# Kernel optimization log

Hardware: AMD Instinct MI355X
Metric: run time of the kernel (lower is better)

The kernel has to match this reference:

```python
import jax, jax.numpy as jnp
import numpy as np

N_QUBITS = 4
N_LAYERS = 2
BATCH = 524288


def _apply_1q(state, U, wire, batched):
    """Apply a 2x2 gate U on `wire`. state: [B,2,2,2,2]; U: [B,2,2] if batched else [2,2]."""
    ax = wire + 1
    s = jnp.moveaxis(state, ax, 1)
    if batched:
        s = jnp.einsum('bij,bj...->bi...', U, s)
    else:
        s = jnp.einsum('ij,bj...->bi...', U, s)
    return jnp.moveaxis(s, 1, ax)


def _apply_cnot(state, control, target):
    cax, tax = control + 1, target + 1
    s0 = jnp.take(state, 0, axis=cax)
    s1 = jnp.take(state, 1, axis=cax)
    t_ax = tax - 1 if tax > cax else tax  # target axis after removing control axis
    s1 = jnp.flip(s1, axis=t_ax)
    return jnp.stack([s0, s1], axis=cax)


def _circuit(x, weight):
    B = x.shape[0]
    # Angle encoding: RY(tanh(x_i) * pi) per wire (per-sample angles)
    theta = jnp.tanh(x) * jnp.pi  # [B, 4]
    state = jnp.zeros((B,) + (2,) * N_QUBITS, jnp.complex64)
    state = state.at[(slice(None),) + (0,) * N_QUBITS].set(1.0)
    for q in range(N_QUBITS):
        h = theta[:, q] * 0.5
        c, s = jnp.cos(h), jnp.sin(h)
        Ury = jnp.stack([jnp.stack([c, -s], -1), jnp.stack([s, c], -1)], -2).astype(jnp.complex64)  # [B,2,2]
        state = _apply_1q(state, Ury, q, batched=True)
    for layer in range(N_LAYERS):
        for q in range(N_QUBITS):
            hy = weight[layer, q, 0] * 0.5
            cy, sy = jnp.cos(hy), jnp.sin(hy)
            Uy = jnp.stack([jnp.stack([cy, -sy]), jnp.stack([sy, cy])]).astype(jnp.complex64)
            state = _apply_1q(state, Uy, q, batched=False)
            hz = weight[layer, q, 1] * 0.5
            ez = jnp.exp(-1j * hz.astype(jnp.complex64))
            z0 = jnp.zeros((), jnp.complex64)
            Uz = jnp.stack([jnp.stack([ez, z0]), jnp.stack([z0, jnp.conj(ez)])])
            state = _apply_1q(state, Uz, q, batched=False)
        for q in range(N_QUBITS):
            state = _apply_cnot(state, q, (q + 1) % N_QUBITS)
    # <Z_i> = P(bit_i = 0) - P(bit_i = 1)
    probs = jnp.abs(state) ** 2  # [B,2,2,2,2] float32
    outs = []
    for q in range(N_QUBITS):
        other_axes = tuple(a for a in range(1, N_QUBITS + 1) if a != q + 1)
        marg = probs.sum(other_axes)  # [B,2]
        outs.append(marg[:, 0] - marg[:, 1])
    return jnp.stack(outs, axis=-1).astype(jnp.float32)  # [B,4]


def setup_inputs() -> dict:
    key = jax.random.key(0)
    kx, kw = jax.random.split(key)
    x = jax.random.normal(kx, (BATCH, N_QUBITS), dtype=jnp.float32)
    weight = jax.random.normal(kw, (N_LAYERS, N_QUBITS, 2), dtype=jnp.float32) * 0.1
    return {"x": x, "weight": weight}


def reference(x, weight):
    return _circuit(x, weight)
```

## Files before the change

kernel.cpp:

```cpp
#include <hip/hip_runtime.h>
#include <math.h>


typedef _Float16 f16x4 __attribute__((ext_vector_type(4)));
typedef _Float16 f16x8 __attribute__((ext_vector_type(8)));
typedef float f32x4 __attribute__((ext_vector_type(4)));

static __device__ inline unsigned pk16(float a, float b) {
    unsigned short ua = __builtin_bit_cast(unsigned short, (_Float16)a);
    unsigned short ub = __builtin_bit_cast(unsigned short, (_Float16)b);
    return (unsigned)ua | ((unsigned)ub << 16);
}

__global__ __launch_bounds__(64) void build_U(
    const float* __restrict__ weight,
    uint2* __restrict__ UF)
{
    __shared__ float cw[16], sw[16];
    __shared__ float Ur[16][16], Ui[16][16];

    const int tid = threadIdx.x;
    if (tid < 16) {
        float h = 0.5f * weight[tid];
        __sincosf(h, &sw[tid], &cw[tid]);
    }
    __syncthreads();

    if (tid < 16) {
        const int col = tid;
        float re[16], im[16];
        #pragma unroll
        for (int i = 0; i < 16; ++i) { re[i] = 0.f; im[i] = 0.f; }
        re[col] = 1.f;

        #pragma unroll
        for (int layer = 0; layer < 2; ++layer) {
            #pragma unroll
            for (int q = 0; q < 4; ++q) {
                float cy = cw[layer*8 + q*2 + 0];
                float sy = sw[layer*8 + q*2 + 0];
                float cz = cw[layer*8 + q*2 + 1];
                float sz = sw[layer*8 + q*2 + 1];
                int st = 8 >> q;
                #pragma unroll
                for (int i = 0; i < 16; ++i) {
                    if (i & st) continue;
                    int j = i | st;
                    float r0 = re[i], r1 = re[j], i0 = im[i], i1 = im[j];
                    float nr0 = cy*r0 - sy*r1;
                    float nr1 = sy*r0 + cy*r1;
                    float ni0 = cy*i0 - sy*i1;
                    float ni1 = sy*i0 + cy*i1;
                    re[i] = nr0*cz + ni0*sz;
                    im[i] = ni0*cz - nr0*sz;
                    re[j] = nr1*cz - ni1*sz;
                    im[j] = ni1*cz + nr1*sz;
                }
            }
            #pragma unroll
            for (int q = 0; q < 4; ++q) {
                int cb = 8 >> q;
                int tb = 8 >> ((q + 1) & 3);
                #pragma unroll
                for (int i = 0; i < 16; ++i) {
                    if ((i & cb) && !(i & tb)) {
                        int j = i | tb;
                        float tr = re[i]; re[i] = re[j]; re[j] = tr;
                        float ti = im[i]; im[i] = im[j]; im[j] = ti;
                    }
                }
            }
        }
        #pragma unroll
        for (int i = 0; i < 16; ++i) { Ur[i][col] = re[i]; Ui[i][col] = im[i]; }
    }
    __syncthreads();

    {
        int m = tid & 15, k0 = (tid >> 4) << 2;
        UF[tid]      = uint2{pk16(Ur[m][k0], Ur[m][k0+1]),
                             pk16(Ur[m][k0+2], Ur[m][k0+3])};
        UF[64 + tid] = uint2{pk16(Ui[m][k0], Ui[m][k0+1]),
                             pk16(Ui[m][k0+2], Ui[m][k0+3])};
    }
}

__global__ __launch_bounds__(256) void qmain(
    const float* __restrict__ x,
    const uint2* __restrict__ UF,
    float* __restrict__ out,
    int B)
{
    __shared__ _Float16 S[256][16];

    const int tid  = threadIdx.x;
    const int lane = tid & 63;
    const int s0   = blockIdx.x * 256 + tid;

    float4 xv = (s0 < B) ? reinterpret_cast<const float4*>(x)[s0]
                         : float4{0.f, 0.f, 0.f, 0.f};

    uint2 ur2 = UF[lane];
    uint2 ui2 = UF[64 + lane];

    float c[4], s[4];
    {
        float xs[4] = {xv.x, xv.y, xv.z, xv.w};
        #pragma unroll
        for (int q = 0; q < 4; ++q) {
            float e = __expf(2.f * xs[q]);
            float uu = __builtin_amdgcn_rcpf(e + 1.f);
            float rr = 0.5f * uu;
            c[q] = __builtin_amdgcn_sinf(rr);
            s[q] = __builtin_amdgcn_cosf(rr);
        }
    }
    float a4[4] = {c[0]*c[1], c[0]*s[1], s[0]*c[1], s[0]*s[1]};
    float b4[4] = {c[2]*c[3], c[2]*s[3], s[2]*c[3], s[2]*s[3]};

    f16x8 lo, hi;
    #pragma unroll
    for (int i = 0; i < 8; ++i)  lo[i] = (_Float16)(a4[i >> 2] * b4[i & 3]);
    #pragma unroll
    for (int i = 8; i < 16; ++i) hi[i - 8] = (_Float16)(a4[i >> 2] * b4[i & 3]);
    *reinterpret_cast<f16x8*>(&S[tid][0]) = lo;
    *reinterpret_cast<f16x8*>(&S[tid][8]) = hi;
    __syncthreads();

    f16x4 afr = __builtin_bit_cast(f16x4, ur2);
    f16x4 afi = __builtin_bit_cast(f16x4, ui2);

    const int lg = lane >> 4;
    const int n  = lane & 15;
    const float sg1 = (lg & 1) ? -1.f : 1.f;
    const float sg0 = (lg & 2) ? -1.f : 1.f;
    const int wrow = tid & 192;
    const int wbase = blockIdx.x * 256 + wrow;

    #pragma unroll
    for (int g = 0; g < 4; ++g) {
        f16x4 bf = *reinterpret_cast<const f16x4*>(&S[wrow + g*16 + n][lg << 2]);

        f32x4 zero = {0.f, 0.f, 0.f, 0.f};
        f32x4 dre = __builtin_amdgcn_mfma_f32_16x16x16f16(afr, bf, zero, 0, 0, 0);
        f32x4 dim = __builtin_amdgcn_mfma_f32_16x16x16f16(afi, bf, zero, 0, 0, 0);

        float m0 = dre[0]*dre[0] + dim[0]*dim[0];
        float m1 = dre[1]*dre[1] + dim[1]*dim[1];
        float m2 = dre[2]*dre[2] + dim[2]*dim[2];
        float m3 = dre[3]*dre[3] + dim[3]*dim[3];

        float sum = (m0 + m1) + (m2 + m3);
        float z3 = (m0 - m1) + (m2 - m3);
        float z2 = (m0 + m1) - (m2 + m3);
        float z1 = sg1 * sum;
        float z0 = sg0 * sum;

        z0 += __shfl_xor(z0, 16); z0 += __shfl_xor(z0, 32);
        z1 += __shfl_xor(z1, 16); z1 += __shfl_xor(z1, 32);
        z2 += __shfl_xor(z2, 16); z2 += __shfl_xor(z2, 32);
        z3 += __shfl_xor(z3, 16); z3 += __shfl_xor(z3, 32);

        int samp = wbase + g*16 + n;
        if (lg == g && samp < B)
            reinterpret_cast<float4*>(out)[samp] = float4{z0, z1, z2, z3};
    }
}

extern "C" void kernel_launch(void* const* d_in, const int* in_sizes, int n_in,
                              void* d_out, int out_size, void* d_ws, size_t ws_size,
                              hipStream_t stream) {
    const float* x = (const float*)d_in[0];
    const float* w = (const float*)d_in[1];
    float* out = (float*)d_out;
    uint2* UF = (uint2*)d_ws;
    int B = in_sizes[0] / 4;

    build_U<<<1, 64, 0, stream>>>(w, UF);
    int grid = (B + 255) / 256;
    qmain<<<grid, 256, 0, stream>>>(x, UF, out, B);
}
```

Before: 68.71 us.

## Fuse unitary build into main kernel and reduce expectations with MFMA

Removes the separate single-block build_U launch, and has every block recompute the 16x16 circuit unitary in LDS from the weights, using 16 threads. The state layout in shared memory becomes column-major f16x4 slabs. The shuffle-based Z-expectation reduction is replaced by a third MFMA against a constant ±1 sign matrix, applied to f16 probabilities. This trades an extra kernel launch and a global round-trip for redundant per-block unitary computation on 16 serial threads, and adds f16 rounding of the probabilities.

```diff
diff --git a/kernel.cpp b/kernel.cpp
--- a/kernel.cpp
+++ b/kernel.cpp
@@ -3,28 +3,49 @@
 
 
 typedef _Float16 f16x4 __attribute__((ext_vector_type(4)));
-typedef _Float16 f16x8 __attribute__((ext_vector_type(8)));
 typedef float f32x4 __attribute__((ext_vector_type(4)));
 
-static __device__ inline unsigned pk16(float a, float b) {
-    unsigned short ua = __builtin_bit_cast(unsigned short, (_Float16)a);
-    unsigned short ub = __builtin_bit_cast(unsigned short, (_Float16)b);
-    return (unsigned)ua | ((unsigned)ub << 16);
-}
+__global__ __launch_bounds__(256, 8) void qfused(
+    const float* __restrict__ x,
+    const float* __restrict__ weight,
+    float* __restrict__ out,
+    int B)
+{
+    __shared__ float Ur[16][16], Ui[16][16];
+    __shared__ f16x4 S2[4][256];
 
-__global__ __launch_bounds__(64) void build_U(
-    const float* __restrict__ weight,
-    uint2* __restrict__ UF)
-{
-    __shared__ float cw[16], sw[16];
-    __shared__ float Ur[16][16], Ui[16][16];
+    const int tid  = threadIdx.x;
+    const int lane = tid & 63;
+    const int s0   = blockIdx.x * 256 + tid;
 
-    const int tid = threadIdx.x;
-    if (tid < 16) {
-        float h = 0.5f * weight[tid];
-        __sincosf(h, &sw[tid], &cw[tid]);
+    float4 xv = (s0 < B) ? reinterpret_cast<const float4*>(x)[s0]
+                         : float4{0.f, 0.f, 0.f, 0.f};
+
+    float c[4], s[4];
+    {
+        float xs[4] = {xv.x, xv.y, xv.z, xv.w};
+        #pragma unroll
+        for (int q = 0; q < 4; ++q) {
+            float e = __expf(2.f * xs[q]);
+            float uu = __builtin_amdgcn_rcpf(e + 1.f);
+            float rr = 0.5f * uu;
+            c[q] = __builtin_amdgcn_sinf(rr);
+            s[q] = __builtin_amdgcn_cosf(rr);
+        }
     }
-    __syncthreads();
+    float a4[4] = {c[0]*c[1], c[0]*s[1], s[0]*c[1], s[0]*s[1]};
+    float b4[4] = {c[2]*c[3], c[2]*s[3], s[2]*c[3], s[2]*s[3]};
+
+    #pragma unroll
+    for (int j = 0; j < 4; ++j) {
+        f16x4 sv;
+        #pragma unroll
+        for (int e = 0; e < 4; ++e) {
+            int i = j*4 + e;
+            sv[e] = (_Float16)(a4[i >> 2] * b4[i & 3]);
+        }
+        S2[j][tid] = sv;
+    }
 
     if (tid < 16) {
         const int col = tid;
@@ -37,10 +58,9 @@
         for (int layer = 0; layer < 2; ++layer) {
             #pragma unroll
             for (int q = 0; q < 4; ++q) {
-                float cy = cw[layer*8 + q*2 + 0];
-                float sy = sw[layer*8 + q*2 + 0];
-                float cz = cw[layer*8 + q*2 + 1];
-                float sz = sw[layer*8 + q*2 + 1];
+                float cy, sy, cz, sz;
+                __sincosf(0.5f * weight[layer*8 + q*2 + 0], &sy, &cy);
+                __sincosf(0.5f * weight[layer*8 + q*2 + 1], &sz, &cz);
                 int st = 8 >> q;
                 #pragma unroll
                 for (int i = 0; i < 16; ++i) {
@@ -76,94 +96,40 @@
     }
     __syncthreads();
 
-    {
-        int m = tid & 15, k0 = (tid >> 4) << 2;
-        UF[tid]      = uint2{pk16(Ur[m][k0], Ur[m][k0+1]),
-                             pk16(Ur[m][k0+2], Ur[m][k0+3])};
-        UF[64 + tid] = uint2{pk16(Ui[m][k0], Ui[m][k0+1]),
-                             pk16(Ui[m][k0+2], Ui[m][k0+3])};
+    const int m  = lane & 15;
+    const int k0 = (lane >> 4) << 2;
+    f16x4 afr, afi, As;
+    #pragma unroll
+    for (int j = 0; j < 4; ++j) {
+        afr[j] = (_Float16)Ur[m][k0 + j];
+        afi[j] = (_Float16)Ui[m][k0 + j];
+        float sgn = (m < 4) ? ((((k0 + j) >> (3 - m)) & 1) ? -1.f : 1.f) : 0.f;
+        As[j] = (_Float16)sgn;
     }
-}
 
-__global__ __launch_bounds__(256) void qmain(
-    const float* __restrict__ x,
-    const uint2* __restrict__ UF,
-    float* __restrict__ out,
-    int B)
-{
-    __shared__ _Float16 S[256][16];
-
-    const int tid  = threadIdx.x;
-    const int lane = tid & 63;
-    const int s0   = blockIdx.x * 256 + tid;
-
-    float4 xv = (s0 < B) ? reinterpret_cast<const float4*>(x)[s0]
-                         : float4{0.f, 0.f, 0.f, 0.f};
-
-    uint2 ur2 = UF[lane];
-    uint2 ui2 = UF[64 + lane];
-
-    float c[4], s[4];
-    {
-        float xs[4] = {xv.x, xv.y, xv.z, xv.w};
-        #pragma unroll
-        for (int q = 0; q < 4; ++q) {
-            float e = __expf(2.f * xs[q]);
-            float uu = __builtin_amdgcn_rcpf(e + 1.f);
-            float rr = 0.5f * uu;
-            c[q] = __builtin_amdgcn_sinf(rr);
-            s[q] = __builtin_amdgcn_cosf(rr);
-        }
-    }
-    float a4[4] = {c[0]*c[1], c[0]*s[1], s[0]*c[1], s[0]*s[1]};
-    float b4[4] = {c[2]*c[3], c[2]*s[3], s[2]*c[3], s[2]*s[3]};
-
-    f16x8 lo, hi;
-    #pragma unroll
-    for (int i = 0; i < 8; ++i)  lo[i] = (_Float16)(a4[i >> 2] * b4[i & 3]);
-    #pragma unroll
-    for (int i = 8; i < 16; ++i) hi[i - 8] = (_Float16)(a4[i >> 2] * b4[i & 3]);
-    *reinterpret_cast<f16x8*>(&S[tid][0]) = lo;
-    *reinterpret_cast<f16x8*>(&S[tid][8]) = hi;
-    __syncthreads();
-
-    f16x4 afr = __builtin_bit_cast(f16x4, ur2);
-    f16x4 afi = __builtin_bit_cast(f16x4, ui2);
-
-    const int lg = lane >> 4;
-    const int n  = lane & 15;
-    const float sg1 = (lg & 1) ? -1.f : 1.f;
-    const float sg0 = (lg & 2) ? -1.f : 1.f;
-    const int wrow = tid & 192;
+    const int n     = lane & 15;
+    const int lg    = lane >> 4;
+    const int wrow  = tid & 192;
     const int wbase = blockIdx.x * 256 + wrow;
 
     #pragma unroll
     for (int g = 0; g < 4; ++g) {
-        f16x4 bf = *reinterpret_cast<const f16x4*>(&S[wrow + g*16 + n][lg << 2]);
+        f16x4 bf = S2[lg][wrow + g*16 + n];
 
         f32x4 zero = {0.f, 0.f, 0.f, 0.f};
         f32x4 dre = __builtin_amdgcn_mfma_f32_16x16x16f16(afr, bf, zero, 0, 0, 0);
         f32x4 dim = __builtin_amdgcn_mfma_f32_16x16x16f16(afi, bf, zero, 0, 0, 0);
 
-        float m0 = dre[0]*dre[0] + dim[0]*dim[0];
-        float m1 = dre[1]*dre[1] + dim[1]*dim[1];
-        float m2 = dre[2]*dre[2] + dim[2]*dim[2];
-        float m3 = dre[3]*dre[3] + dim[3]*dim[3];
+        f16x4 mb;
+        #pragma unroll
+        for (int r = 0; r < 4; ++r)
+            mb[r] = (_Float16)(dre[r]*dre[r] + dim[r]*dim[r]);
 
-        float sum = (m0 + m1) + (m2 + m3);
-        float z3 = (m0 - m1) + (m2 - m3);
-        float z2 = (m0 + m1) - (m2 + m3);
-        float z1 = sg1 * sum;
-        float z0 = sg0 * sum;
+        f32x4 zv = __builtin_amdgcn_mfma_f32_16x16x16f16(As, mb, zero, 0, 0, 0);
 
-        z0 += __shfl_xor(z0, 16); z0 += __shfl_xor(z0, 32);
-        z1 += __shfl_xor(z1, 16); z1 += __shfl_xor(z1, 32);
-        z2 += __shfl_xor(z2, 16); z2 += __shfl_xor(z2, 32);
-        z3 += __shfl_xor(z3, 16); z3 += __shfl_xor(z3, 32);
-
-        int samp = wbase + g*16 + n;
-        if (lg == g && samp < B)
-            reinterpret_cast<float4*>(out)[samp] = float4{z0, z1, z2, z3};
+        int samp = wbase + g*16 + lane;
+        if (lane < 16 && samp < B)
+            reinterpret_cast<float4*>(out)[samp] = float4{zv[0], zv[1], zv[2], zv[3]};
     }
 }
 
@@ -173,10 +139,8 @@
     const float* x = (const float*)d_in[0];
     const float* w = (const float*)d_in[1];
     float* out = (float*)d_out;
-    uint2* UF = (uint2*)d_ws;
     int B = in_sizes[0] / 4;
 
-    build_U<<<1, 64, 0, stream>>>(w, UF);
     int grid = (B + 255) / 256;
-    qmain<<<grid, 256, 0, stream>>>(x, UF, out, B);
+    qfused<<<grid, 256, 0, stream>>>(x, w, out, B);
 }
```

Measured after the change: 66.51 us. 1.03x faster.
